# Kernel tuning notes

Measured on AMD Instinct MI355X. Metric: run time of the kernel, lower is better.

The kernel has to match this reference:

```python
import jax, jax.numpy as jnp
import numpy as np

ITERATIONS = 3
EPS = 1e-06

def squash(s):
    # square_norm along last dim, keepdims (matches torch squash)
    sq = jnp.sum(s * s, axis=-1, keepdims=True)
    return sq / (1.0 + sq) * s / (jnp.sqrt(sq) + EPS)

def setup_inputs() -> dict:
    key = jax.random.key(0)
    k1, k2 = jax.random.split(key)
    x = jax.random.normal(k1, (64, 32, 8, 8, 16), dtype=jnp.float32)
    W = jax.random.normal(k2, (1, 32, 8, 8, 32, 16, 32), dtype=jnp.float32)
    return {"x": x, "W": W}

def reference(x, W):
    # u_hat: (B, C, H, Wd, O, D) = x (B,C,H,Wd,I) @ W (C,H,Wd,O,I,D)
    u_hat = jnp.einsum('bchwi,chwoid->bchwod', x, W[0])
    b = jnp.zeros(u_hat.shape[:-1], dtype=u_hat.dtype)  # (B,C,H,Wd,O)
    for _ in range(ITERATIONS - 1):
        c = jax.nn.softmax(b, axis=-1)
        s = jnp.sum(c[..., None] * u_hat, axis=(1, 2, 3))  # (B,O,D)
        v = squash(s)
        b = b + jnp.sum(u_hat * v[:, None, None, None], axis=-1)
    c = jax.nn.softmax(b, axis=-1)
    s = jnp.sum(c[..., None] * u_hat, axis=(1, 2, 3))
    return squash(s)  # (B, out_capsules, out_cap_dim)
```

## Files before the change

kernel.cpp:

```cpp
#include <hip/hip_runtime.h>
#include <math.h>

#define B_ 64
#define N_ 2048
#define O_ 32
#define I_ 16
#define D_ 32
#define OD_ 1024

typedef __attribute__((ext_vector_type(8))) short bf16x8;
typedef __attribute__((ext_vector_type(4))) float f32x4;

union FragU { unsigned u[4]; uint4 v; bf16x8 f; };

__device__ __forceinline__ void barrier_lds() {
  asm volatile("s_waitcnt lgkmcnt(0)\n\ts_barrier" ::: "memory");
}

template <int CTRL>
__device__ __forceinline__ float dpp_mov_f(float x) {
  return __int_as_float(
      __builtin_amdgcn_update_dpp(0, __float_as_int(x), CTRL, 0xf, 0xf, true));
}
__device__ __forceinline__ float grp32_max(float x) {
  x = fmaxf(x, dpp_mov_f<0xb1>(x));
  x = fmaxf(x, dpp_mov_f<0x4e>(x));
  x = fmaxf(x, dpp_mov_f<0x124>(x));
  x = fmaxf(x, dpp_mov_f<0x128>(x));
  x = fmaxf(x, __shfl_xor(x, 16));
  return x;
}
__device__ __forceinline__ float grp32_sum(float x) {
  x += dpp_mov_f<0xb1>(x);
  x += dpp_mov_f<0x4e>(x);
  x += dpp_mov_f<0x124>(x);
  x += dpp_mov_f<0x128>(x);
  x += __shfl_xor(x, 16);
  return x;
}

__device__ __forceinline__ void dk_split(float f, unsigned &h, unsigned &l) {
  unsigned u = __float_as_uint(f);
  h = u & 0xffff0000u;
  float lo = f - __uint_as_float(h);
  l = __float_as_uint(lo) >> 16;
}
__device__ __forceinline__ void dk_split16(float f, unsigned short &h,
                                           unsigned short &l) {
  unsigned u = __float_as_uint(f);
  unsigned hu = u & 0xffff0000u;
  h = (unsigned short)(u >> 16);
  float lo = f - __uint_as_float(hu);
  l = (unsigned short)(__float_as_uint(lo) >> 16);
}
__device__ __forceinline__ unsigned pk(unsigned short e0, unsigned short e1) {
  return (unsigned)e0 | ((unsigned)e1 << 16);
}

__global__ __launch_bounds__(256) void prep_x(const float* __restrict__ x,
                                              uint4* __restrict__ XP) {
  const int tid = threadIdx.x;
  int t = blockIdx.x * 256 + tid;
  int c = t & 15, n = (t >> 4) & 2047, bg = t >> 15;
  const f32x4* xq = (const f32x4*)(x + ((size_t)(bg * 16 + c) * N_ + n) * I_);
  float xv[I_];
#pragma unroll
  for (int k = 0; k < 4; ++k) {
    f32x4 q4 = __builtin_nontemporal_load(xq + k);
    xv[4 * k + 0] = q4[0];
    xv[4 * k + 1] = q4[1];
    xv[4 * k + 2] = q4[2];
    xv[4 * k + 3] = q4[3];
  }
  unsigned short hh[I_], ll[I_];
#pragma unroll
  for (int i = 0; i < I_; ++i) dk_split16(xv[i], hh[i], ll[i]);
  size_t base = ((size_t)bg * N_ + n) * 4;
#pragma unroll
  for (int sel = 0; sel < 2; ++sel) {
    const unsigned short* e = sel ? ll : hh;
#pragma unroll
    for (int qp = 0; qp < 2; ++qp) {
      uint4 u;
      u.x = pk(e[qp * 8 + 0], e[qp * 8 + 1]);
      u.y = pk(e[qp * 8 + 2], e[qp * 8 + 3]);
      u.z = pk(e[qp * 8 + 4], e[qp * 8 + 5]);
      u.w = pk(e[qp * 8 + 6], e[qp * 8 + 7]);
      XP[(base + sel * 2 + qp) * 16 + c] = u;
    }
  }
}

__global__ __launch_bounds__(1024, 4) void pass1_fused(
    const uint4* __restrict__ XP, const float* __restrict__ W,
    uint4* __restrict__ WP, float* __restrict__ partial, int NC) {
  const int tid = threadIdx.x;
  const int lane = tid & 63;
  const int w = tid >> 6;
  const int q = lane >> 4;
  const int c = lane & 15;
  const int qp = q & 1;
  const int ch = blockIdx.x;
  const int bgy = blockIdx.y;

  __shared__ uint4 xps[2][16][4][16];
  __shared__ float wstage[16][1024];

  const int n0 = ch * NC;

  {
    uint4* xf = (uint4*)xps;
    const int total = 2 * NC * 64;
    for (int l = tid; l < total; l += 1024) {
      int bgl = l / (NC * 64);
      int rest = l - bgl * (NC * 64);
      xf[bgl * 1024 + rest] =
          XP[(size_t)(bgy * 2 + bgl) * 131072 + (size_t)n0 * 64 + rest];
    }
  }

  f32x4 s_t[2][4];
#pragma unroll
  for (int bgl = 0; bgl < 2; ++bgl)
#pragma unroll
    for (int ct = 0; ct < 4; ++ct) s_t[bgl][ct] = (f32x4){0.f, 0.f, 0.f, 0.f};

  const float* wsrc = W + (size_t)(2 * w) * 512;
  f32x4* ws4 = (f32x4*)wstage[w];
  const float* ws = wstage[w];

  f32x4 wreg[4];
  {
    const f32x4* g = (const f32x4*)(wsrc + (size_t)n0 * 16384);
#pragma unroll
    for (int k = 0; k < 4; ++k) wreg[k] = g[lane + k * 64];
#pragma unroll
    for (int k = 0; k < 4; ++k) ws4[lane + k * 64] = wreg[k];
  }

  barrier_lds();

  for (int nl = 0; nl < NC; ++nl) {
    const size_t n = (size_t)(n0 + nl);
    const size_t np = (nl + 1 < NC) ? n + 1 : n;
    {
      const f32x4* g = (const f32x4*)(wsrc + np * 16384);
#pragma unroll
      for (int k = 0; k < 4; ++k) wreg[k] = g[lane + k * 64];
    }
    FragU cb[4];
#pragma unroll
    for (int ct = 0; ct < 4; ++ct) {
      const int ol = ct >> 1, dh = ct & 1;
      const float* base = ws + ol * 512 + qp * 256 + dh * 16 + c;
      unsigned short e8[8];
#pragma unroll
      for (int e = 0; e < 8; ++e) {
        float f = base[e * 32];
        unsigned u = __float_as_uint(f);
        unsigned short hi = (unsigned short)(u >> 16);
        unsigned short lo = (unsigned short)(
            __float_as_uint(f - __uint_as_float(u & 0xffff0000u)) >> 16);
        e8[e] = (q < 2) ? hi : lo;
      }
      cb[ct].u[0] = pk(e8[0], e8[1]);
      cb[ct].u[1] = pk(e8[2], e8[3]);
      cb[ct].u[2] = pk(e8[4], e8[5]);
      cb[ct].u[3] = pk(e8[6], e8[7]);
    }
    if (bgy == 0) {
      uint4* wpdst = WP + n * 4096 + (size_t)(2 * w) * 128 + lane;
#pragma unroll
      for (int ct = 0; ct < 4; ++ct) wpdst[ct * 64] = cb[ct].v;
    }
#pragma unroll
    for (int bgl = 0; bgl < 2; ++bgl) {
      FragU ah, al;
      ah.v = xps[bgl][nl][qp][c];
      al.v = xps[bgl][nl][2 + qp][c];
#pragma unroll
      for (int ct = 0; ct < 4; ++ct) {
        s_t[bgl][ct] = __builtin_amdgcn_mfma_f32_16x16x32_bf16(
            ah.f, cb[ct].f, s_t[bgl][ct], 0, 0, 0);
        s_t[bgl][ct] = __builtin_amdgcn_mfma_f32_16x16x32_bf16(
            al.f, cb[ct].f, s_t[bgl][ct], 0, 0, 0);
      }
    }
#pragma unroll
    for (int k = 0; k < 4; ++k) ws4[lane + k * 64] = wreg[k];
  }

  const float scale = 1.f / 32.f;
#pragma unroll
  for (int bgl = 0; bgl < 2; ++bgl)
#pragma unroll
    for (int ct = 0; ct < 4; ++ct) {
      int odc = (2 * w + (ct >> 1)) * 32 + (ct & 1) * 16 + c;
#pragma unroll
      for (int r = 0; r < 4; ++r) {
        partial[((size_t)ch * B_ + bgy * 32 + bgl * 16 + q * 4 + r) * OD_ + odc] =
            s_t[bgl][ct][r] * scale;
      }
    }
}

template <int UNIFORM>
__global__ __launch_bounds__(1024, 4) void mfma_pass6(
    const uint4* __restrict__ XP, const uint4* __restrict__ WP,
    const float* __restrict__ v, float* __restrict__ partial, int NC) {
  const int tid = threadIdx.x;
  const int lane = tid & 63;
  const int w = tid >> 6;
  const int q = lane >> 4;
  const int c = lane & 15;
  const int qp = q & 1;
  const int ch = blockIdx.x;
  const int bgy = blockIdx.y;

  __shared__ uint4 xps[2][16][4][16];
  __shared__ float ls_l[32 * 33];
  __shared__ float ls_c2[32 * 33];

  const int n0 = ch * NC;

  {
    uint4* xf = (uint4*)xps;
    const int total = 2 * NC * 64;
    for (int l = tid; l < total; l += 1024) {
      int bgl = l / (NC * 64);
      int rest = l - bgl * (NC * 64);
      xf[bgl * 1024 + rest] =
          XP[(size_t)(bgy * 2 + bgl) * 131072 + (size_t)n0 * 64 + rest];
    }
  }

  f32x4 s_t[2][4];
#pragma unroll
  for (int bgl = 0; bgl < 2; ++bgl)
#pragma unroll
    for (int ct = 0; ct < 4; ++ct) s_t[bgl][ct] = (f32x4){0.f, 0.f, 0.f, 0.f};

  float vreg[2][4][4];
  if (!UNIFORM) {
#pragma unroll
    for (int bgl = 0; bgl < 2; ++bgl)
#pragma unroll
      for (int ct = 0; ct < 4; ++ct) {
        const float4 vv = *(const float4*)&v[(size_t)(bgy * 32 + bgl * 16 + c) * OD_ +
                                             (2 * w + (ct >> 1)) * 32 +
                                             (ct & 1) * 16 + q * 4];
        vreg[bgl][ct][0] = vv.x;
        vreg[bgl][ct][1] = vv.y;
        vreg[bgl][ct][2] = vv.z;
        vreg[bgl][ct][3] = vv.w;
      }
  }

  barrier_lds();

  const uint4* wbase = WP + (size_t)(2 * w) * 128 + lane;

  FragU cb[4];
#pragma unroll
  for (int ct = 0; ct < 4; ++ct)
    cb[ct].v = wbase[(size_t)n0 * 4096 + ct * 64];

  if (UNIFORM) {
    for (int nl = 0; nl < NC; ++nl) {
      const size_t n = (size_t)(n0 + nl);
      const size_t np = (nl + 1 < NC) ? n + 1 : n;
      FragU cbn[4];
#pragma unroll
      for (int ct = 0; ct < 4; ++ct) cbn[ct].v = wbase[np * 4096 + ct * 64];
#pragma unroll
      for (int bgl = 0; bgl < 2; ++bgl) {
        FragU ah, al;
        ah.v = xps[bgl][nl][qp][c];
        al.v = xps[bgl][nl][2 + qp][c];
#pragma unroll
        for (int ct = 0; ct < 4; ++ct) {
          s_t[bgl][ct] = __builtin_amdgcn_mfma_f32_16x16x32_bf16(
              ah.f, cb[ct].f, s_t[bgl][ct], 0, 0, 0);
          s_t[bgl][ct] = __builtin_amdgcn_mfma_f32_16x16x32_bf16(
              al.f, cb[ct].f, s_t[bgl][ct], 0, 0, 0);
        }
      }
#pragma unroll
      for (int ct = 0; ct < 4; ++ct) cb[ct] = cbn[ct];
    }
  } else {
    for (int nl = 0; nl < NC; ++nl) {
      const size_t n = (size_t)(n0 + nl);
      const size_t np = (nl + 1 < NC) ? n + 1 : n;

#pragma unroll
      for (int bgl = 0; bgl < 2; ++bgl) {
        FragU ah, al;
        ah.v = xps[bgl][nl][qp][c];
        al.v = xps[bgl][nl][2 + qp][c];
        float lgol[2] = {0.f, 0.f};
#pragma unroll
        for (int ct = 0; ct < 4; ++ct) {
          f32x4 accT = (f32x4){0.f, 0.f, 0.f, 0.f};
          accT = __builtin_amdgcn_mfma_f32_16x16x32_bf16(cb[ct].f, ah.f, accT, 0, 0, 0);
          f32x4 uT = __builtin_amdgcn_mfma_f32_16x16x32_bf16(cb[ct].f, al.f, accT, 0, 0, 0);
          const int ol = ct >> 1;
#pragma unroll
          for (int r = 0; r < 4; ++r)
            lgol[ol] = fmaf(uT[r], vreg[bgl][ct][r], lgol[ol]);
        }
#pragma unroll
        for (int ol = 0; ol < 2; ++ol) {
          float t = lgol[ol];
          t += __shfl_xor(t, 16);
          t += __shfl_xor(t, 32);
          if (q == 0) ls_l[(2 * w + ol) * 33 + bgl * 16 + c] = t;
        }
      }
      FragU cbn[4];
#pragma unroll
      for (int ct = 0; ct < 4; ++ct) cbn[ct].v = wbase[np * 4096 + ct * 64];

      barrier_lds();
      {
        const int idx = (tid & 31) * 33 + (tid >> 5);
        float l = ls_l[idx];
        float mx = grp32_max(l);
        float e = __expf(l - mx);
        float sm = grp32_sum(e);
        ls_c2[idx] = e / sm;
      }
      barrier_lds();
#pragma unroll
      for (int bgl = 0; bgl < 2; ++bgl) {
        FragU ah, al;
        ah.v = xps[bgl][nl][qp][c];
        al.v = xps[bgl][nl][2 + qp][c];
#pragma unroll
        for (int ct = 0; ct < 4; ++ct) {
          f32x4 acc = (f32x4){0.f, 0.f, 0.f, 0.f};
          acc = __builtin_amdgcn_mfma_f32_16x16x32_bf16(ah.f, cb[ct].f, acc, 0, 0, 0);
          f32x4 u = __builtin_amdgcn_mfma_f32_16x16x32_bf16(al.f, cb[ct].f, acc, 0, 0, 0);
          const int o = 2 * w + (ct >> 1);
#pragma unroll
          for (int r = 0; r < 4; ++r) {
            float cc = ls_c2[o * 33 + bgl * 16 + q * 4 + r];
            s_t[bgl][ct][r] = fmaf(cc, u[r], s_t[bgl][ct][r]);
          }
        }
      }
#pragma unroll
      for (int ct = 0; ct < 4; ++ct) cb[ct] = cbn[ct];
    }
  }

  const float scale = UNIFORM ? (1.f / 32.f) : 1.f;
#pragma unroll
  for (int bgl = 0; bgl < 2; ++bgl)
#pragma unroll
    for (int ct = 0; ct < 4; ++ct) {
      int odc = (2 * w + (ct >> 1)) * 32 + (ct & 1) * 16 + c;
#pragma unroll
      for (int r = 0; r < 4; ++r) {
        partial[((size_t)ch * B_ + bgy * 32 + bgl * 16 + q * 4 + r) * OD_ + odc] =
            s_t[bgl][ct][r] * scale;
      }
    }
}

template <int UNIFORM>
__global__ __launch_bounds__(512, 4) void mfma_pass_fb(
    const float* __restrict__ x, const float* __restrict__ W,
    const float* __restrict__ v, float* __restrict__ partial, int NC) {
  const int tid = threadIdx.x;
  const int lane = tid & 63;
  const int cg = tid >> 6;
  const int q = lane >> 4;
  const int c = lane & 15;
  const int ch = blockIdx.x;
  const int bg = blockIdx.y;

  __shared__ float ls_logit[16 * O_];
  __shared__ float ls_c[16 * O_];

  f32x4 s_t[8];
#pragma unroll
  for (int ct = 0; ct < 8; ++ct) s_t[ct] = (f32x4){0.f, 0.f, 0.f, 0.f};

  const int n0 = ch * NC;
  const int ih = (q & 1) * 8;
  const float* xrow = x + ((size_t)(bg * 16 + c) * N_) * I_ + ih;

  for (int nl = 0; nl < NC; ++nl) {
    const int n = n0 + nl;
    const float* xp = xrow + (size_t)n * I_;
    float4 xv0 = *(const float4*)xp;
    float4 xv1 = *(const float4*)(xp + 4);
    float xv[8] = {xv0.x, xv0.y, xv0.z, xv0.w, xv1.x, xv1.y, xv1.z, xv1.w};
    FragU a1;
#pragma unroll
    for (int p = 0; p < 4; ++p) {
      unsigned h0, l0, h1, l1;
      dk_split(xv[2 * p], h0, l0);
      dk_split(xv[2 * p + 1], h1, l1);
      a1.u[p] = (q < 2) ? ((h0 >> 16) | h1) : (l0 | (l1 << 16));
    }
    f32x4 u_t[8];
#pragma unroll
    for (int ct = 0; ct < 8; ++ct) {
      const int o = cg * 4 + (ct >> 1);
      const int d = (ct & 1) * 16 + c;
      const float* wp = W + (((size_t)n * O_ + o) * I_ + ih) * D_ + d;
      FragU b1, b2;
#pragma unroll
      for (int p = 0; p < 4; ++p) {
        unsigned h0, l0, h1, l1;
        dk_split(wp[(2 * p) * D_], h0, l0);
        dk_split(wp[(2 * p + 1) * D_], h1, l1);
        b1.u[p] = (h0 >> 16) | h1;
        b2.u[p] = l0 | (l1 << 16);
      }
      if (UNIFORM) {
        s_t[ct] = __builtin_amdgcn_mfma_f32_16x16x32_bf16(a1.f, b1.f, s_t[ct], 0, 0, 0);
        s_t[ct] = __builtin_amdgcn_mfma_f32_16x16x32_bf16(a1.f, b2.f, s_t[ct], 0, 0, 0);
      } else {
        f32x4 acc = (f32x4){0.f, 0.f, 0.f, 0.f};
        acc = __builtin_amdgcn_mfma_f32_16x16x32_bf16(a1.f, b1.f, acc, 0, 0, 0);
        u_t[ct] = __builtin_amdgcn_mfma_f32_16x16x32_bf16(a1.f, b2.f, acc, 0, 0, 0);
      }
    }
    if (!UNIFORM) {
#pragma unroll
      for (int ol = 0; ol < 4; ++ol) {
        float lg[4] = {0.f, 0.f, 0.f, 0.f};
#pragma unroll
        for (int hf = 0; hf < 2; ++hf) {
          int ct = ol * 2 + hf;
          int odc = cg * 128 + ct * 16 + c;
#pragma unroll
          for (int r = 0; r < 4; ++r)
            lg[r] = fmaf(u_t[ct][r], v[(size_t)(bg * 16 + q * 4 + r) * OD_ + odc], lg[r]);
        }
#pragma unroll
        for (int r = 0; r < 4; ++r) {
#pragma unroll
          for (int m = 1; m < 16; m <<= 1) lg[r] += __shfl_xor(lg[r], m);
        }
        if (c == 0) {
#pragma unroll
          for (int r = 0; r < 4; ++r)
            ls_logit[(q * 4 + r) * O_ + cg * 4 + ol] = lg[r];
        }
      }
      __syncthreads();
      {
        int b_l = tid >> 5, o = tid & 31;
        float l = ls_logit[b_l * O_ + o];
        float mx = l;
#pragma unroll
        for (int m = 16; m >= 1; m >>= 1) mx = fmaxf(mx, __shfl_xor(mx, m));
        float e = __expf(l - mx);
        float sm = e;
#pragma unroll
        for (int m = 16; m >= 1; m >>= 1) sm += __shfl_xor(sm, m);
        ls_c[b_l * O_ + o] = e / sm;
      }
      __syncthreads();
#pragma unroll
      for (int ol = 0; ol < 4; ++ol) {
        int o = cg * 4 + ol;
        float cc[4];
#pragma unroll
        for (int r = 0; r < 4; ++r) cc[r] = ls_c[(q * 4 + r) * O_ + o];
#pragma unroll
        for (int hf = 0; hf < 2; ++hf) {
          int ct = ol * 2 + hf;
#pragma unroll
          for (int r = 0; r < 4; ++r)
            s_t[ct][r] = fmaf(cc[r], u_t[ct][r], s_t[ct][r]);
        }
      }
    }
  }

  const float scale = UNIFORM ? (1.f / 32.f) : 1.f;
#pragma unroll
  for (int ct = 0; ct < 8; ++ct) {
#pragma unroll
    for (int r = 0; r < 4; ++r) {
      partial[((size_t)ch * B_ + bg * 16 + q * 4 + r) * OD_ + cg * 128 + ct * 16 + c] =
          s_t[ct][r] * scale;
    }
  }
}

__global__ __launch_bounds__(256) void reduce_fused(
    const float4* __restrict__ part, int cq4, const float4* __restrict__ prev,
    float4* __restrict__ out) {
  __shared__ float4 accs[4][64];
  const int lane = threadIdx.x & 63;
  const int cg = threadIdx.x >> 6;
  const int g4 = blockIdx.x * 64 + lane;
  float4 s = make_float4(0.f, 0.f, 0.f, 0.f);
  const int c0 = cg * cq4;
  for (int i = 0; i < cq4; ++i) {
    float4 p = part[(size_t)(c0 + i) * 16384 + g4];
    s.x += p.x; s.y += p.y; s.z += p.z; s.w += p.w;
  }
  accs[cg][lane] = s;
  __syncthreads();
  if (cg == 0) {
    float4 a1 = accs[1][lane], a2 = accs[2][lane], a3 = accs[3][lane];
    s.x += a1.x + a2.x + a3.x;
    s.y += a1.y + a2.y + a3.y;
    s.z += a1.z + a2.z + a3.z;
    s.w += a1.w + a2.w + a3.w;
    float sq = s.x * s.x + s.y * s.y + s.z * s.z + s.w * s.w;
#pragma unroll
    for (int m = 4; m >= 1; m >>= 1) sq += __shfl_xor(sq, m, 8);
    float scale = sq / ((1.f + sq) * (sqrtf(sq) + 1e-6f));
    float4 r = make_float4(s.x * scale, s.y * scale, s.z * scale, s.w * scale);
    if (prev) {
      float4 p = prev[g4];
      r.x += p.x; r.y += p.y; r.z += p.z; r.w += p.w;
    }
    out[g4] = r;
  }
}

__global__ __launch_bounds__(256) void reduce_squash(
    const float4* __restrict__ part, int chunks,
    const float4* __restrict__ prev, float4* __restrict__ out) {
  int g4 = blockIdx.x * 256 + threadIdx.x;
  float4 s = make_float4(0.f, 0.f, 0.f, 0.f);
#pragma unroll 4
  for (int ch = 0; ch < chunks; ++ch) {
    float4 p = part[(size_t)ch * 16384 + g4];
    s.x += p.x; s.y += p.y; s.z += p.z; s.w += p.w;
  }
  float sq = s.x * s.x + s.y * s.y + s.z * s.z + s.w * s.w;
#pragma unroll
  for (int m = 4; m >= 1; m >>= 1) sq += __shfl_xor(sq, m, 8);
  float scale = sq / ((1.f + sq) * (sqrtf(sq) + 1e-6f));
  float4 r = make_float4(s.x * scale, s.y * scale, s.z * scale, s.w * scale);
  if (prev) {
    float4 p = prev[g4];
    r.x += p.x; r.y += p.y; r.z += p.z; r.w += p.w;
  }
  out[g4] = r;
}

extern "C" void kernel_launch(void* const* d_in, const int* in_sizes, int n_in,
                              void* d_out, int out_size, void* d_ws,
                              size_t ws_size, hipStream_t stream) {
  const float* x = (const float*)d_in[0];
  const float* W = (const float*)d_in[1];
  float* out = (float*)d_out;

  const size_t XP_FLOATS = 4ull * 2048 * 4 * 16 * 4;
  const size_t WP_FLOATS = 2048ull * 32 * 2 * 4 * 16 * 4;

  float* v1 = (float*)d_ws;
  float* vsum = v1 + 65536;
  float* partial = vsum + 65536;

  const int chunks = 128;
  bool packed_path =
      (131072 + (size_t)chunks * 65536 + XP_FLOATS + WP_FLOATS) * 4 <= ws_size;

  if (packed_path) {
    uint4* XP = (uint4*)(partial + (size_t)chunks * 65536);
    uint4* WP = XP + XP_FLOATS / 4;
    const int NC = N_ / chunks;
    const int cq4 = chunks / 4;
    dim3 grid(chunks, 2);

    prep_x<<<512, 256, 0, stream>>>(x, XP);

    pass1_fused<<<grid, 1024, 0, stream>>>(XP, W, WP, partial, NC);
    reduce_fused<<<256, 256, 0, stream>>>((const float4*)partial, cq4, nullptr,
                                          (float4*)v1);
    mfma_pass6<0><<<grid, 1024, 0, stream>>>(XP, WP, v1, partial, NC);
    reduce_fused<<<256, 256, 0, stream>>>((const float4*)partial, cq4,
                                          (const float4*)v1, (float4*)vsum);
    mfma_pass6<0><<<grid, 1024, 0, stream>>>(XP, WP, vsum, partial, NC);
    reduce_fused<<<256, 256, 0, stream>>>((const float4*)partial, cq4, nullptr,
                                          (float4*)out);
  } else {
    int fchunks = 128;
    while (fchunks > 1 && (131072 + (size_t)fchunks * 65536) * 4 > ws_size)
      fchunks >>= 1;
    int NC = N_ / fchunks;
    dim3 grid(fchunks, 4);

    mfma_pass_fb<1><<<grid, 512, 0, stream>>>(x, W, nullptr, partial, NC);
    reduce_squash<<<64, 256, 0, stream>>>((const float4*)partial, fchunks,
                                          nullptr, (float4*)v1);
    mfma_pass_fb<0><<<grid, 512, 0, stream>>>(x, W, v1, partial, NC);
    reduce_squash<<<64, 256, 0, stream>>>((const float4*)partial, fchunks,
                                          (const float4*)v1, (float4*)vsum);
    mfma_pass_fb<0><<<grid, 512, 0, stream>>>(x, W, vsum, partial, NC);
    reduce_squash<<<64, 256, 0, stream>>>((const float4*)partial, fchunks,
                                          nullptr, (float4*)out);
  }
}
```

Measured before the change: 359.4 us.

## Double-buffer W staging in pass1 and read X fragments directly from global

Pass1 now keeps two LDS buffers for W so that the next slice is written while the current one is read. Global loads are prefetched two steps ahead using nontemporal loads. The up-front LDS staging of the X fragments is removed, and the fragments are loaded straight from global memory each step. The loop is unrolled by two to alternate buffers. This is meant to hide W load latency and drop the initial X copy, but LDS use doubles for W and there is more global traffic for X. The paired unrolling also assumes NC is even, and each wave stages and reads only its own W slice without any barrier.

New measurement: 369.5 us. 2.8% more time.

```diff
diff --git a/kernel.cpp b/kernel.cpp
--- a/kernel.cpp
+++ b/kernel.cpp
@@ -103,22 +103,10 @@
   const int ch = blockIdx.x;
   const int bgy = blockIdx.y;
 
-  __shared__ uint4 xps[2][16][4][16];
-  __shared__ float wstage[16][1024];
+  __shared__ float wstage[2][16][1024];
 
   const int n0 = ch * NC;
 
-  {
-    uint4* xf = (uint4*)xps;
-    const int total = 2 * NC * 64;
-    for (int l = tid; l < total; l += 1024) {
-      int bgl = l / (NC * 64);
-      int rest = l - bgl * (NC * 64);
-      xf[bgl * 1024 + rest] =
-          XP[(size_t)(bgy * 2 + bgl) * 131072 + (size_t)n0 * 64 + rest];
-    }
-  }
-
   f32x4 s_t[2][4];
 #pragma unroll
   for (int bgl = 0; bgl < 2; ++bgl)
@@ -126,69 +114,83 @@
     for (int ct = 0; ct < 4; ++ct) s_t[bgl][ct] = (f32x4){0.f, 0.f, 0.f, 0.f};
 
   const float* wsrc = W + (size_t)(2 * w) * 512;
-  f32x4* ws4 = (f32x4*)wstage[w];
-  const float* ws = wstage[w];
-
-  f32x4 wreg[4];
+  const uint4* xb0 = XP + (size_t)(bgy * 2 + 0) * 131072;
+  const uint4* xb1 = XP + (size_t)(bgy * 2 + 1) * 131072;
+
+  f32x4* wb0 = (f32x4*)wstage[0][w];
+  f32x4* wb1 = (f32x4*)wstage[1][w];
+  const float* wr0 = wstage[0][w];
+  const float* wr1 = wstage[1][w];
+
+  f32x4 wA[4], wB[4];
   {
     const f32x4* g = (const f32x4*)(wsrc + (size_t)n0 * 16384);
 #pragma unroll
-    for (int k = 0; k < 4; ++k) wreg[k] = g[lane + k * 64];
-#pragma unroll
-    for (int k = 0; k < 4; ++k) ws4[lane + k * 64] = wreg[k];
-  }
-
-  barrier_lds();
-
-  for (int nl = 0; nl < NC; ++nl) {
-    const size_t n = (size_t)(n0 + nl);
-    const size_t np = (nl + 1 < NC) ? n + 1 : n;
-    {
-      const f32x4* g = (const f32x4*)(wsrc + np * 16384);
-#pragma unroll
-      for (int k = 0; k < 4; ++k) wreg[k] = g[lane + k * 64];
-    }
-    FragU cb[4];
-#pragma unroll
-    for (int ct = 0; ct < 4; ++ct) {
-      const int ol = ct >> 1, dh = ct & 1;
-      const float* base = ws + ol * 512 + qp * 256 + dh * 16 + c;
-      unsigned short e8[8];
-#pragma unroll
-      for (int e = 0; e < 8; ++e) {
-        float f = base[e * 32];
-        unsigned u = __float_as_uint(f);
-        unsigned short hi = (unsigned short)(u >> 16);
-        unsigned short lo = (unsigned short)(
-            __float_as_uint(f - __uint_as_float(u & 0xffff0000u)) >> 16);
-        e8[e] = (q < 2) ? hi : lo;
-      }
-      cb[ct].u[0] = pk(e8[0], e8[1]);
-      cb[ct].u[1] = pk(e8[2], e8[3]);
-      cb[ct].u[2] = pk(e8[4], e8[5]);
-      cb[ct].u[3] = pk(e8[6], e8[7]);
-    }
-    if (bgy == 0) {
-      uint4* wpdst = WP + n * 4096 + (size_t)(2 * w) * 128 + lane;
-#pragma unroll
-      for (int ct = 0; ct < 4; ++ct) wpdst[ct * 64] = cb[ct].v;
-    }
-#pragma unroll
-    for (int bgl = 0; bgl < 2; ++bgl) {
-      FragU ah, al;
-      ah.v = xps[bgl][nl][qp][c];
-      al.v = xps[bgl][nl][2 + qp][c];
-#pragma unroll
-      for (int ct = 0; ct < 4; ++ct) {
-        s_t[bgl][ct] = __builtin_amdgcn_mfma_f32_16x16x32_bf16(
-            ah.f, cb[ct].f, s_t[bgl][ct], 0, 0, 0);
-        s_t[bgl][ct] = __builtin_amdgcn_mfma_f32_16x16x32_bf16(
-            al.f, cb[ct].f, s_t[bgl][ct], 0, 0, 0);
-      }
-    }
-#pragma unroll
-    for (int k = 0; k < 4; ++k) ws4[lane + k * 64] = wreg[k];
-  }
+    for (int k = 0; k < 4; ++k)
+      wA[k] = __builtin_nontemporal_load(g + lane + k * 64);
+#pragma unroll
+    for (int k = 0; k < 4; ++k) wb0[lane + k * 64] = wA[k];
+    const f32x4* g1 = (const f32x4*)(wsrc + (size_t)(n0 + 1) * 16384);
+#pragma unroll
+    for (int k = 0; k < 4; ++k)
+      wA[k] = __builtin_nontemporal_load(g1 + lane + k * 64);
+  }
+
+#define P1_BODY(NL, WREAD, WWRITE, WRIN, WROUT)                               \
+  {                                                                           \
+    const int nl_ = (NL);                                                     \
+    const size_t n_ = (size_t)(n0 + nl_);                                     \
+    const int nn_ = (nl_ + 2 < NC) ? nl_ + 2 : NC - 1;                        \
+    const f32x4* g_ = (const f32x4*)(wsrc + (size_t)(n0 + nn_) * 16384);      \
+    _Pragma("unroll") for (int k = 0; k < 4; ++k)                             \
+        WROUT[k] = __builtin_nontemporal_load(g_ + lane + k * 64);            \
+    FragU ah0, al0, ah1, al1;                                                 \
+    ah0.v = xb0[n_ * 64 + qp * 16 + c];                                       \
+    al0.v = xb0[n_ * 64 + (2 + qp) * 16 + c];                                 \
+    ah1.v = xb1[n_ * 64 + qp * 16 + c];                                       \
+    al1.v = xb1[n_ * 64 + (2 + qp) * 16 + c];                                 \
+    _Pragma("unroll") for (int k = 0; k < 4; ++k)                             \
+        WWRITE[lane + k * 64] = WRIN[k];                                      \
+    FragU cb[4];                                                              \
+    _Pragma("unroll") for (int ct = 0; ct < 4; ++ct) {                        \
+      const int ol_ = ct >> 1, dh_ = ct & 1;                                  \
+      const float* base_ = WREAD + ol_ * 512 + qp * 256 + dh_ * 16 + c;       \
+      unsigned short e8[8];                                                   \
+      _Pragma("unroll") for (int e = 0; e < 8; ++e) {                         \
+        float f_ = base_[e * 32];                                             \
+        unsigned u_ = __float_as_uint(f_);                                    \
+        unsigned short hi_ = (unsigned short)(u_ >> 16);                      \
+        unsigned short lo_ = (unsigned short)(                                \
+            __float_as_uint(f_ - __uint_as_float(u_ & 0xffff0000u)) >> 16);   \
+        e8[e] = (q < 2) ? hi_ : lo_;                                          \
+      }                                                                       \
+      cb[ct].u[0] = pk(e8[0], e8[1]);                                         \
+      cb[ct].u[1] = pk(e8[2], e8[3]);                                         \
+      cb[ct].u[2] = pk(e8[4], e8[5]);                                         \
+      cb[ct].u[3] = pk(e8[6], e8[7]);                                         \
+    }                                                                         \
+    if (bgy == 0) {                                                           \
+      uint4* wpdst_ = WP + n_ * 4096 + (size_t)(2 * w) * 128 + lane;          \
+      _Pragma("unroll") for (int ct = 0; ct < 4; ++ct)                        \
+          wpdst_[ct * 64] = cb[ct].v;                                         \
+    }                                                                         \
+    _Pragma("unroll") for (int ct = 0; ct < 4; ++ct) {                        \
+      s_t[0][ct] = __builtin_amdgcn_mfma_f32_16x16x32_bf16(ah0.f, cb[ct].f,   \
+                                                           s_t[0][ct], 0, 0, 0); \
+      s_t[0][ct] = __builtin_amdgcn_mfma_f32_16x16x32_bf16(al0.f, cb[ct].f,   \
+                                                           s_t[0][ct], 0, 0, 0); \
+      s_t[1][ct] = __builtin_amdgcn_mfma_f32_16x16x32_bf16(ah1.f, cb[ct].f,   \
+                                                           s_t[1][ct], 0, 0, 0); \
+      s_t[1][ct] = __builtin_amdgcn_mfma_f32_16x16x32_bf16(al1.f, cb[ct].f,   \
+                                                           s_t[1][ct], 0, 0, 0); \
+    }                                                                         \
+  }
+
+  for (int nl = 0; nl < NC; nl += 2) {
+    P1_BODY(nl, wr0, wb1, wA, wB);
+    P1_BODY(nl + 1, wr1, wb0, wB, wA);
+  }
+#undef P1_BODY
 
   const float scale = 1.f / 32.f;
 #pragma unroll
```
